# Kernel optimization log

Hardware: AMD Instinct MI355X
Metric: run time of the kernel (lower is better)

## Reference

```python
import jax, jax.numpy as jnp
import numpy as np

N_NODES = 50000
N_EDGES = 1_600_000
D_IN = 128
D_HID = 128
N_CLASSES = 8
N_GRAPHS = 64


def setup_inputs() -> dict:
    key = jax.random.key(0)
    ks = jax.random.split(key, 8)
    x = jax.random.normal(ks[0], (N_NODES, D_IN), dtype=jnp.float32)
    edge_index = jax.random.randint(ks[1], (2, N_EDGES), 0, N_NODES, dtype=jnp.int32)
    graph_ids = jnp.sort(jax.random.randint(ks[2], (N_NODES,), 0, N_GRAPHS, dtype=jnp.int32))
    s = 1.0 / np.sqrt(D_HID)
    W1 = jax.random.normal(ks[3], (D_IN, D_HID), dtype=jnp.float32) * s
    b1 = jnp.zeros((D_HID,), dtype=jnp.float32)
    W2 = jax.random.normal(ks[4], (D_HID, D_HID), dtype=jnp.float32) * s
    b2 = jnp.zeros((D_HID,), dtype=jnp.float32)
    Wc = jax.random.normal(ks[5], (D_HID, N_CLASSES), dtype=jnp.float32) * s
    bc = jnp.zeros((N_CLASSES,), dtype=jnp.float32)
    return {"x": x, "edge_index": edge_index, "graph_ids": graph_ids,
            "W1": W1, "b1": b1, "W2": W2, "b2": b2, "Wc": Wc, "bc": bc}


def _gcn_layer(h, src, dst, norm, W, b):
    # message: gather source features, apply symmetric degree normalization
    msg = h[src] * norm[:, None]                       # [E, d]
    agg = jax.ops.segment_sum(msg, dst, num_segments=N_NODES)  # [N, d]
    return jax.nn.relu(agg @ W + b)


def reference(x, edge_index, graph_ids, W1, b1, W2, b2, Wc, bc):
    src, dst = edge_index[0], edge_index[1]
    ones_e = jnp.ones((N_EDGES,), dtype=x.dtype)
    deg = jax.ops.segment_sum(ones_e, dst, num_segments=N_NODES)
    deg_inv_sqrt = jnp.where(deg > 0, jax.lax.rsqrt(jnp.maximum(deg, 1.0)), 0.0)
    norm = deg_inv_sqrt[src] * deg_inv_sqrt[dst]       # [E]

    h = _gcn_layer(x, src, dst, norm, W1, b1)
    h = _gcn_layer(h, src, dst, norm, W2, b2)

    # per-graph mean pooling (segment mean over nodes of each graph)
    ones_n = jnp.ones((N_NODES,), dtype=h.dtype)
    counts = jax.ops.segment_sum(ones_n, graph_ids, num_segments=N_GRAPHS)
    pooled = jax.ops.segment_sum(h, graph_ids, num_segments=N_GRAPHS)
    pooled = pooled / jnp.maximum(counts, 1.0)[:, None]  # [G, d]

    logits = pooled @ Wc + bc                           # [G, n_classes]
    return logits
```

## Files before the change

### kernel.cpp

```cpp
#include <hip/hip_runtime.h>
#include <hip/hip_bf16.h>

#define D_HID 128
#define N_GRAPHS 64
#define N_CLASSES 8
#define NPB 16
#define CAP 96
#define KSWEEP 4


__device__ inline unsigned short f2b(float x) {
    unsigned int u = __float_as_uint(x);
    unsigned int r = (u + 0x7fffu + ((u >> 16) & 1u)) >> 16;
    return (unsigned short)r;
}
__device__ inline float b2f(unsigned short u) {
    return __uint_as_float((unsigned int)u << 16);
}

__global__ __launch_bounds__(256) void prep_kernel(const float* __restrict__ x,
                                                   uint2* __restrict__ xb4,
                                                   int castBlocks, int n4,
                                                   const int* __restrict__ src,
                                                   const int* __restrict__ dst,
                                                   int* __restrict__ cursor,
                                                   unsigned short* __restrict__ csr16,
                                                   int E, int N, int fillBlocks, int rangeSize) {
    const int b = blockIdx.x;
    if (b < castBlocks) {
        int i = b * 256 + threadIdx.x;
        if (i < n4) {
            float4 v = ((const float4*)x)[i];
            uint2 o;
            o.x = (unsigned int)f2b(v.x) | ((unsigned int)f2b(v.y) << 16);
            o.y = (unsigned int)f2b(v.z) | ((unsigned int)f2b(v.w) << 16);
            xb4[i] = o;
        }
        return;
    }
    const int fb = b - castBlocks;
    const int sweep = fb / fillBlocks;
    const int blk = fb - sweep * fillBlocks;
    const int e = blk * 256 + threadIdx.x;
    if (e >= E) return;
    const int s = src[e];
    const int lo = sweep * rangeSize;
    if (s < lo || s >= lo + rangeSize) return;
    const int d = dst[e];
    int slot = atomicAdd(&cursor[d], 1);
    if (slot < CAP) csr16[(size_t)slot * N + d] = (unsigned short)s;
}

__global__ __launch_bounds__(256) void dis_counts_kernel(const int* __restrict__ deg,
                                                         float* __restrict__ dis,
                                                         const int* __restrict__ gid,
                                                         int* __restrict__ counts, int N) {
    int n = blockIdx.x * blockDim.x + threadIdx.x;
    if (n < N) {
        int v = deg[n];
        dis[n] = (v > 0) ? rsqrtf((float)v) : 0.0f;
    }
    if (blockIdx.x == 0 && threadIdx.x < N_GRAPHS) {
        int g = threadIdx.x;
        int lo0 = 0, hi0 = N;
        while (lo0 < hi0) { int mid = (lo0 + hi0) >> 1; if (gid[mid] < g) lo0 = mid + 1; else hi0 = mid; }
        int lo1 = lo0, hi1 = N;
        while (lo1 < hi1) { int mid = (lo1 + hi1) >> 1; if (gid[mid] < g + 1) lo1 = mid + 1; else hi1 = mid; }
        counts[g] = lo1 - lo0;
    }
}

__global__ __launch_bounds__(256) void layer_kernel(const unsigned short* __restrict__ h_in,
                                                    const int* __restrict__ deg,
                                                    const unsigned short* __restrict__ csr16,
                                                    const float* __restrict__ dis,
                                                    const float* __restrict__ W,
                                                    const float* __restrict__ bias,
                                                    unsigned short* __restrict__ h_out,
                                                    float* __restrict__ pooled,
                                                    const int* __restrict__ gid,
                                                    int fuse_pool, int N) {
    const int base = blockIdx.x * NPB;
    const int tid = threadIdx.x;
    const int wv = tid >> 6;
    const int lane = tid & 63;
    const int q = lane >> 4;
    const int ql = lane & 15;
    __shared__ float s_agg[NPB][D_HID];

    const int n0 = base + wv * 4;
    float acc[4][8] = {};
    int dd[4];
    #pragma unroll
    for (int i = 0; i < 4; ++i) {
        const int n = n0 + i;
        dd[i] = (n < N) ? min(deg[n], CAP) : 0;
    }
    const int dm = max(max(dd[0], dd[1]), max(dd[2], dd[3]));

    for (int cb = 0; cb < dm; cb += 64) {
        const int cm = min(64, dm - cb);
        unsigned int pk[4];
        #pragma unroll
        for (int i = 0; i < 4; ++i) {
            pk[i] = 0u;
            if (lane < dd[i] - cb) {
                unsigned int u = (unsigned int)csr16[(size_t)(cb + lane) * N + (n0 + i)];
                pk[i] = u | ((unsigned int)f2b(dis[u]) << 16);
            }
        }
        #pragma unroll 4
        for (int j = 0; j < cm; j += 4) {
            const int e = j + q;
            #pragma unroll
            for (int i = 0; i < 4; ++i) {
                const unsigned int p = (unsigned int)__shfl((int)pk[i], e);
                const float w = __uint_as_float(p & 0xffff0000u);
                const uint4 r = *(const uint4*)&h_in[(size_t)(p & 0xffffu) * D_HID + ql * 8];
                acc[i][0] = fmaf(w, __uint_as_float(r.x << 16), acc[i][0]);
                acc[i][1] = fmaf(w, __uint_as_float(r.x & 0xffff0000u), acc[i][1]);
                acc[i][2] = fmaf(w, __uint_as_float(r.y << 16), acc[i][2]);
                acc[i][3] = fmaf(w, __uint_as_float(r.y & 0xffff0000u), acc[i][3]);
                acc[i][4] = fmaf(w, __uint_as_float(r.z << 16), acc[i][4]);
                acc[i][5] = fmaf(w, __uint_as_float(r.z & 0xffff0000u), acc[i][5]);
                acc[i][6] = fmaf(w, __uint_as_float(r.w << 16), acc[i][6]);
                acc[i][7] = fmaf(w, __uint_as_float(r.w & 0xffff0000u), acc[i][7]);
            }
        }
    }

    #pragma unroll
    for (int i = 0; i < 4; ++i) {
        #pragma unroll
        for (int k = 0; k < 8; ++k) {
            acc[i][k] += __shfl_down(acc[i][k], 32);
            acc[i][k] += __shfl_down(acc[i][k], 16);
        }
        if (q == 0) {
            const float dn = (n0 + i < N) ? dis[n0 + i] : 0.0f;
            #pragma unroll
            for (int k = 0; k < 8; ++k) s_agg[wv * 4 + i][ql * 8 + k] = acc[i][k] * dn;
        }
    }
    __syncthreads();

    const int t = tid & 127;
    const int nb = tid >> 7;
    float outv[8];
    const float bt = bias[t];
    #pragma unroll
    for (int i = 0; i < 8; ++i) outv[i] = bt;

    for (int k = 0; k < D_HID; k += 4) {
        const float w0 = W[(k + 0) * D_HID + t];
        const float w1 = W[(k + 1) * D_HID + t];
        const float w2 = W[(k + 2) * D_HID + t];
        const float w3 = W[(k + 3) * D_HID + t];
        #pragma unroll
        for (int i = 0; i < 8; ++i) {
            float4 a = *(const float4*)&s_agg[nb * 8 + i][k];
            outv[i] = fmaf(a.x, w0, outv[i]);
            outv[i] = fmaf(a.y, w1, outv[i]);
            outv[i] = fmaf(a.z, w2, outv[i]);
            outv[i] = fmaf(a.w, w3, outv[i]);
        }
    }

    #pragma unroll
    for (int i = 0; i < 8; ++i) {
        const int n = base + nb * 8 + i;
        if (n >= N) break;
        float v = fmaxf(outv[i], 0.0f);
        if (fuse_pool) {
            atomicAdd(&pooled[gid[n] * D_HID + t], v);
        } else {
            h_out[(size_t)n * D_HID + t] = f2b(v);
        }
    }
}

__global__ __launch_bounds__(128) void pool_kernel(const unsigned short* __restrict__ h,
                                                   const int* __restrict__ gid,
                                                   float* __restrict__ pooled,
                                                   int N, int nodes_per_block) {
    const int t = threadIdx.x;
    const int start = blockIdx.x * nodes_per_block;
    if (start >= N) return;
    const int endn = min(start + nodes_per_block, N);
    int cur = gid[start];
    float sum = 0.0f;
    for (int n = start; n < endn; ++n) {
        int g = gid[n];
        if (g != cur) {
            atomicAdd(&pooled[cur * D_HID + t], sum);
            cur = g; sum = 0.0f;
        }
        sum += b2f(h[(size_t)n * D_HID + t]);
    }
    atomicAdd(&pooled[cur * D_HID + t], sum);
}

__global__ __launch_bounds__(512) void classify_kernel(const float* __restrict__ pooled,
                                                       const int* __restrict__ counts,
                                                       const float* __restrict__ Wc,
                                                       const float* __restrict__ bc,
                                                       float* __restrict__ out) {
    const int g = threadIdx.x >> 3;
    const int c = threadIdx.x & 7;
    float inv = 1.0f / fmaxf((float)counts[g], 1.0f);
    float acc = bc[c];
    #pragma unroll 8
    for (int k = 0; k < D_HID; ++k) {
        acc = fmaf(pooled[g * D_HID + k] * inv, Wc[k * N_CLASSES + c], acc);
    }
    out[g * N_CLASSES + c] = acc;
}

extern "C" void kernel_launch(void* const* d_in, const int* in_sizes, int n_in,
                              void* d_out, int out_size, void* d_ws, size_t ws_size,
                              hipStream_t stream) {
    const float* x   = (const float*)d_in[0];
    const int* edge  = (const int*)d_in[1];
    const int* gid   = (const int*)d_in[2];
    const float* W1  = (const float*)d_in[3];
    const float* b1  = (const float*)d_in[4];
    const float* W2  = (const float*)d_in[5];
    const float* b2  = (const float*)d_in[6];
    const float* Wc  = (const float*)d_in[7];
    const float* bc  = (const float*)d_in[8];
    float* out       = (float*)d_out;

    const int E = in_sizes[1] / 2;
    const int N = in_sizes[2];
    const int* src = edge;
    const int* dst = edge + E;

    char* p = (char*)d_ws;
    auto take = [&](size_t bytes) {
        char* r = p;
        p += (bytes + 255) & ~(size_t)255;
        return r;
    };
    int*   cursor  = (int*)take((size_t)N * 4);
    float* dis     = (float*)take((size_t)N * 4);
    float* pooled  = (float*)take((size_t)N_GRAPHS * D_HID * 4);
    int*   counts  = (int*)take((size_t)N_GRAPHS * 4);
    unsigned short* csr16 = (unsigned short*)take((size_t)N * CAP * 2);
    unsigned short* xb  = (unsigned short*)take((size_t)N * D_HID * 2);
    unsigned short* h1b = (unsigned short*)take((size_t)N * D_HID * 2);
    size_t used = (size_t)(p - (char*)d_ws);
    size_t h2_bytes = (size_t)N * D_HID * 2;
    const bool separate_pool = (used + h2_bytes <= ws_size);
    unsigned short* h2b = separate_pool ? (unsigned short*)take(h2_bytes) : nullptr;

    hipMemsetAsync(cursor, 0, (size_t)N * 4, stream);
    hipMemsetAsync(pooled, 0, (size_t)N_GRAPHS * D_HID * 4, stream);

    const int EB = 256;
    const int n4 = (N * D_HID) / 4;
    const int castBlocks = (n4 + EB - 1) / EB;
    const int fillBlocks = (E + EB - 1) / EB;
    const int rangeSize = (N + KSWEEP - 1) / KSWEEP;
    prep_kernel<<<castBlocks + KSWEEP * fillBlocks, EB, 0, stream>>>(
        x, (uint2*)xb, castBlocks, n4, src, dst, cursor, csr16, E, N, fillBlocks, rangeSize);
    dis_counts_kernel<<<(N + EB - 1) / EB, EB, 0, stream>>>(cursor, dis, gid, counts, N);

    const int LG = (N + NPB - 1) / NPB;
    layer_kernel<<<LG, 256, 0, stream>>>(xb, cursor, csr16, dis, W1, b1, h1b, pooled, gid, 0, N);

    if (separate_pool) {
        layer_kernel<<<LG, 256, 0, stream>>>(h1b, cursor, csr16, dis, W2, b2, h2b, pooled, gid, 0, N);
        const int NPBLK = 8;
        pool_kernel<<<(N + NPBLK - 1) / NPBLK, 128, 0, stream>>>(h2b, gid, pooled, N, NPBLK);
    } else {
        layer_kernel<<<LG, 256, 0, stream>>>(h1b, cursor, csr16, dis, W2, b2, nullptr, pooled, gid, 1, N);
    }

    classify_kernel<<<1, 512, 0, stream>>>(pooled, counts, Wc, bc, out);
}
```

Measured before the change: 343.1 us.

## Partition CSR build by destination per XCD, switch to row-major CSR, persistent layer grid

```diff
diff --git a/kernel.cpp b/kernel.cpp
--- a/kernel.cpp
+++ b/kernel.cpp
@@ -6,7 +6,9 @@
 #define N_CLASSES 8
 #define NPB 16
 #define CAP 96
-#define KSWEEP 4
+#define KSWEEP 2
+#define NXCD 8
+#define LGRID 2048
 
 
 __device__ inline unsigned short f2b(float x) {
@@ -25,7 +27,8 @@
                                                    const int* __restrict__ dst,
                                                    int* __restrict__ cursor,
                                                    unsigned short* __restrict__ csr16,
-                                                   int E, int N, int fillBlocks, int rangeSize) {
+                                                   int E, int N, int fillBlocks,
+                                                   int srcRange, int dstRange) {
     const int b = blockIdx.x;
     if (b < castBlocks) {
         int i = b * 256 + threadIdx.x;
@@ -39,16 +42,37 @@
         return;
     }
     const int fb = b - castBlocks;
-    const int sweep = fb / fillBlocks;
-    const int blk = fb - sweep * fillBlocks;
-    const int e = blk * 256 + threadIdx.x;
-    if (e >= E) return;
-    const int s = src[e];
-    const int lo = sweep * rangeSize;
-    if (s < lo || s >= lo + rangeSize) return;
-    const int d = dst[e];
-    int slot = atomicAdd(&cursor[d], 1);
-    if (slot < CAP) csr16[(size_t)slot * N + d] = (unsigned short)s;
+    const int per_sweep = fillBlocks * NXCD;
+    const int sweep = fb / per_sweep;
+    const int within = fb - sweep * per_sweep;
+    const int chunk = within >> 3;
+    const int part  = b & 7;
+    const int t = chunk * 256 + threadIdx.x;
+    const int e0 = t * 4;
+    if (e0 >= E) return;
+    const int dlo = part * dstRange;
+    const int slo = sweep * srcRange;
+    if (e0 + 3 < E) {
+        const int4 d4 = ((const int4*)dst)[t];
+        #pragma unroll
+        for (int k = 0; k < 4; ++k) {
+            const int d = (&d4.x)[k];
+            if ((unsigned)(d - dlo) >= (unsigned)dstRange) continue;
+            const int s = src[e0 + k];
+            if ((unsigned)(s - slo) >= (unsigned)srcRange) continue;
+            const int slot = atomicAdd(&cursor[d], 1);
+            if (slot < CAP) csr16[(size_t)d * CAP + slot] = (unsigned short)s;
+        }
+    } else {
+        for (int k = 0; e0 + k < E; ++k) {
+            const int d = dst[e0 + k];
+            if ((unsigned)(d - dlo) >= (unsigned)dstRange) continue;
+            const int s = src[e0 + k];
+            if ((unsigned)(s - slo) >= (unsigned)srcRange) continue;
+            const int slot = atomicAdd(&cursor[d], 1);
+            if (slot < CAP) csr16[(size_t)d * CAP + slot] = (unsigned short)s;
+        }
+    }
 }
 
 __global__ __launch_bounds__(256) void dis_counts_kernel(const int* __restrict__ deg,
@@ -79,103 +103,106 @@
                                                     unsigned short* __restrict__ h_out,
                                                     float* __restrict__ pooled,
                                                     const int* __restrict__ gid,
-                                                    int fuse_pool, int N) {
-    const int base = blockIdx.x * NPB;
+                                                    int fuse_pool, int nGroups, int N) {
     const int tid = threadIdx.x;
     const int wv = tid >> 6;
     const int lane = tid & 63;
     const int q = lane >> 4;
     const int ql = lane & 15;
+    const int t = tid & 127;
+    const int nb = tid >> 7;
     __shared__ float s_agg[NPB][D_HID];
 
-    const int n0 = base + wv * 4;
-    float acc[4][8] = {};
-    int dd[4];
-    #pragma unroll
-    for (int i = 0; i < 4; ++i) {
-        const int n = n0 + i;
-        dd[i] = (n < N) ? min(deg[n], CAP) : 0;
-    }
-    const int dm = max(max(dd[0], dd[1]), max(dd[2], dd[3]));
-
-    for (int cb = 0; cb < dm; cb += 64) {
-        const int cm = min(64, dm - cb);
-        unsigned int pk[4];
+    for (int grp = blockIdx.x; grp < nGroups; grp += gridDim.x) {
+        const int base = grp * NPB;
+        const int n0 = base + wv * 4;
+        float acc[4][8] = {};
+        int dd[4];
         #pragma unroll
         for (int i = 0; i < 4; ++i) {
-            pk[i] = 0u;
-            if (lane < dd[i] - cb) {
-                unsigned int u = (unsigned int)csr16[(size_t)(cb + lane) * N + (n0 + i)];
-                pk[i] = u | ((unsigned int)f2b(dis[u]) << 16);
-            }
-        }
-        #pragma unroll 4
-        for (int j = 0; j < cm; j += 4) {
-            const int e = j + q;
+            const int n = n0 + i;
+            dd[i] = (n < N) ? min(deg[n], CAP) : 0;
+        }
+        const int dm = max(max(dd[0], dd[1]), max(dd[2], dd[3]));
+
+        for (int cb = 0; cb < dm; cb += 64) {
+            const int cm = min(64, dm - cb);
+            unsigned int pk[4];
             #pragma unroll
             for (int i = 0; i < 4; ++i) {
-                const unsigned int p = (unsigned int)__shfl((int)pk[i], e);
-                const float w = __uint_as_float(p & 0xffff0000u);
-                const uint4 r = *(const uint4*)&h_in[(size_t)(p & 0xffffu) * D_HID + ql * 8];
-                acc[i][0] = fmaf(w, __uint_as_float(r.x << 16), acc[i][0]);
-                acc[i][1] = fmaf(w, __uint_as_float(r.x & 0xffff0000u), acc[i][1]);
-                acc[i][2] = fmaf(w, __uint_as_float(r.y << 16), acc[i][2]);
-                acc[i][3] = fmaf(w, __uint_as_float(r.y & 0xffff0000u), acc[i][3]);
-                acc[i][4] = fmaf(w, __uint_as_float(r.z << 16), acc[i][4]);
-                acc[i][5] = fmaf(w, __uint_as_float(r.z & 0xffff0000u), acc[i][5]);
-                acc[i][6] = fmaf(w, __uint_as_float(r.w << 16), acc[i][6]);
-                acc[i][7] = fmaf(w, __uint_as_float(r.w & 0xffff0000u), acc[i][7]);
-            }
-        }
-    }
-
-    #pragma unroll
-    for (int i = 0; i < 4; ++i) {
-        #pragma unroll
-        for (int k = 0; k < 8; ++k) {
-            acc[i][k] += __shfl_down(acc[i][k], 32);
-            acc[i][k] += __shfl_down(acc[i][k], 16);
-        }
-        if (q == 0) {
-            const float dn = (n0 + i < N) ? dis[n0 + i] : 0.0f;
+                pk[i] = 0u;
+                if (lane < dd[i] - cb) {
+                    unsigned int u = (unsigned int)csr16[(size_t)(n0 + i) * CAP + cb + lane];
+                    pk[i] = u | ((unsigned int)f2b(dis[u]) << 16);
+                }
+            }
+            #pragma unroll 4
+            for (int j = 0; j < cm; j += 4) {
+                const int e = j + q;
+                #pragma unroll
+                for (int i = 0; i < 4; ++i) {
+                    const unsigned int p = (unsigned int)__shfl((int)pk[i], e);
+                    const float w = __uint_as_float(p & 0xffff0000u);
+                    const uint4 r = *(const uint4*)&h_in[(size_t)(p & 0xffffu) * D_HID + ql * 8];
+                    acc[i][0] = fmaf(w, __uint_as_float(r.x << 16), acc[i][0]);
+                    acc[i][1] = fmaf(w, __uint_as_float(r.x & 0xffff0000u), acc[i][1]);
+                    acc[i][2] = fmaf(w, __uint_as_float(r.y << 16), acc[i][2]);
+                    acc[i][3] = fmaf(w, __uint_as_float(r.y & 0xffff0000u), acc[i][3]);
+                    acc[i][4] = fmaf(w, __uint_as_float(r.z << 16), acc[i][4]);
+                    acc[i][5] = fmaf(w, __uint_as_float(r.z & 0xffff0000u), acc[i][5]);
+                    acc[i][6] = fmaf(w, __uint_as_float(r.w << 16), acc[i][6]);
+                    acc[i][7] = fmaf(w, __uint_as_float(r.w & 0xffff0000u), acc[i][7]);
+                }
+            }
+        }
+
+        #pragma unroll
+        for (int i = 0; i < 4; ++i) {
             #pragma unroll
-            for (int k = 0; k < 8; ++k) s_agg[wv * 4 + i][ql * 8 + k] = acc[i][k] * dn;
-        }
-    }
-    __syncthreads();
-
-    const int t = tid & 127;
-    const int nb = tid >> 7;
-    float outv[8];
-    const float bt = bias[t];
-    #pragma unroll
-    for (int i = 0; i < 8; ++i) outv[i] = bt;
-
-    for (int k = 0; k < D_HID; k += 4) {
-        const float w0 = W[(k + 0) * D_HID + t];
-        const float w1 = W[(k + 1) * D_HID + t];
-        const float w2 = W[(k + 2) * D_HID + t];
-        const float w3 = W[(k + 3) * D_HID + t];
+            for (int k = 0; k < 8; ++k) {
+                acc[i][k] += __shfl_down(acc[i][k], 32);
+                acc[i][k] += __shfl_down(acc[i][k], 16);
+            }
+            if (q == 0) {
+                const float dn = (n0 + i < N) ? dis[n0 + i] : 0.0f;
+                #pragma unroll
+                for (int k = 0; k < 8; ++k) s_agg[wv * 4 + i][ql * 8 + k] = acc[i][k] * dn;
+            }
+        }
+        __syncthreads();
+
+        float outv[8];
+        const float bt = bias[t];
+        #pragma unroll
+        for (int i = 0; i < 8; ++i) outv[i] = bt;
+
+        for (int k = 0; k < D_HID; k += 4) {
+            const float w0 = W[(k + 0) * D_HID + t];
+            const float w1 = W[(k + 1) * D_HID + t];
+            const float w2 = W[(k + 2) * D_HID + t];
+            const float w3 = W[(k + 3) * D_HID + t];
+            #pragma unroll
+            for (int i = 0; i < 8; ++i) {
+                float4 a = *(const float4*)&s_agg[nb * 8 + i][k];
+                outv[i] = fmaf(a.x, w0, outv[i]);
+                outv[i] = fmaf(a.y, w1, outv[i]);
+                outv[i] = fmaf(a.z, w2, outv[i]);
+                outv[i] = fmaf(a.w, w3, outv[i]);
+            }
+        }
+
         #pragma unroll
         for (int i = 0; i < 8; ++i) {
-            float4 a = *(const float4*)&s_agg[nb * 8 + i][k];
-            outv[i] = fmaf(a.x, w0, outv[i]);
-            outv[i] = fmaf(a.y, w1, outv[i]);
-            outv[i] = fmaf(a.z, w2, outv[i]);
-            outv[i] = fmaf(a.w, w3, outv[i]);
-        }
-    }
-
-    #pragma unroll
-    for (int i = 0; i < 8; ++i) {
-        const int n = base + nb * 8 + i;
-        if (n >= N) break;
-        float v = fmaxf(outv[i], 0.0f);
-        if (fuse_pool) {
-            atomicAdd(&pooled[gid[n] * D_HID + t], v);
-        } else {
-            h_out[(size_t)n * D_HID + t] = f2b(v);
-        }
+            const int n = base + nb * 8 + i;
+            if (n >= N) break;
+            float v = fmaxf(outv[i], 0.0f);
+            if (fuse_pool) {
+                atomicAdd(&pooled[gid[n] * D_HID + t], v);
+            } else {
+                h_out[(size_t)n * D_HID + t] = f2b(v);
+            }
+        }
+        __syncthreads();
     }
 }
 
@@ -259,21 +286,23 @@
     const int EB = 256;
     const int n4 = (N * D_HID) / 4;
     const int castBlocks = (n4 + EB - 1) / EB;
-    const int fillBlocks = (E + EB - 1) / EB;
-    const int rangeSize = (N + KSWEEP - 1) / KSWEEP;
-    prep_kernel<<<castBlocks + KSWEEP * fillBlocks, EB, 0, stream>>>(
-        x, (uint2*)xb, castBlocks, n4, src, dst, cursor, csr16, E, N, fillBlocks, rangeSize);
+    const int fillBlocks = ((E + 3) / 4 + EB - 1) / EB;
+    const int srcRange = (N + KSWEEP - 1) / KSWEEP;
+    const int dstRange = (N + NXCD - 1) / NXCD;
+    prep_kernel<<<castBlocks + KSWEEP * NXCD * fillBlocks, EB, 0, stream>>>(
+        x, (uint2*)xb, castBlocks, n4, src, dst, cursor, csr16, E, N, fillBlocks, srcRange, dstRange);
     dis_counts_kernel<<<(N + EB - 1) / EB, EB, 0, stream>>>(cursor, dis, gid, counts, N);
 
-    const int LG = (N + NPB - 1) / NPB;
-    layer_kernel<<<LG, 256, 0, stream>>>(xb, cursor, csr16, dis, W1, b1, h1b, pooled, gid, 0, N);
+    const int nGroups = (N + NPB - 1) / NPB;
+    const int LG = nGroups < LGRID ? nGroups : LGRID;
+    layer_kernel<<<LG, 256, 0, stream>>>(xb, cursor, csr16, dis, W1, b1, h1b, pooled, gid, 0, nGroups, N);
 
     if (separate_pool) {
-        layer_kernel<<<LG, 256, 0, stream>>>(h1b, cursor, csr16, dis, W2, b2, h2b, pooled, gid, 0, N);
+        layer_kernel<<<LG, 256, 0, stream>>>(h1b, cursor, csr16, dis, W2, b2, h2b, pooled, gid, 0, nGroups, N);
         const int NPBLK = 8;
         pool_kernel<<<(N + NPBLK - 1) / NPBLK, 128, 0, stream>>>(h2b, gid, pooled, N, NPBLK);
     } else {
-        layer_kernel<<<LG, 256, 0, stream>>>(h1b, cursor, csr16, dis, W2, b2, nullptr, pooled, gid, 1, N);
+        layer_kernel<<<LG, 256, 0, stream>>>(h1b, cursor, csr16, dis, W2, b2, nullptr, pooled, gid, 1, nGroups, N);
     }
 
     classify_kernel<<<1, 512, 0, stream>>>(pooled, counts, Wc, bc, out);
```

Measured after the change: 399.8 us. +16.5%, slower.
